# Performance work log

Measured on AMD Instinct MI355X. Metric: run time of the kernel, lower is better.

## Reference

```python
import jax, jax.numpy as jnp
import numpy as np

OUT_F, IN_F = 11008, 4096
GROUP_SIZE = 128
NUM_GROUPS = IN_F // GROUP_SIZE  # 32


def setup_inputs() -> dict:
    key = jax.random.key(0)
    k1, k2, k3, k4 = jax.random.split(key, 4)
    x = jax.random.normal(k1, (2, 2048, IN_F), dtype=jnp.float32)
    # signed 4-bit RTN codes in [-8, 7]
    qweight = jax.random.randint(k2, (OUT_F, IN_F), 0, 16, dtype=jnp.int32) - 8
    # per-group scales (out_features, in_features // group_size)
    scales = jax.random.uniform(k3, (OUT_F, NUM_GROUPS), dtype=jnp.float32) * 0.02 + 1e-3
    bias = jax.random.normal(k4, (OUT_F,), dtype=jnp.float32) * 0.01
    return {"x": x, "qweight": qweight, "scales": scales, "bias": bias}


def reference(x, qweight, scales, bias):
    # RTN dequant: w[o, i] = qweight[o, i] * scales[o, i // group_size]
    w = (qweight.astype(x.dtype).reshape(OUT_F, NUM_GROUPS, GROUP_SIZE)
         * scales[:, :, None]).reshape(OUT_F, IN_F)
    # y = x @ w.T + bias  -> [batch, seq, out_features]
    return jnp.einsum('bsi,oi->bso', x, w) + bias
```

## Files before the change

### kernel.cpp

```cpp
#include <hip/hip_runtime.h>

#define OUT_F 11008
#define IN_F  4096
#define M_TOT 4096
#define BM    256
#define BN    256
#define BK    64
#define NKT   (IN_F / BK)
#define TM_N  (M_TOT / BM)
#define TN_N  (OUT_F / BN)
#define NWG   (TM_N * TN_N)

typedef __bf16 bf16;
typedef __attribute__((ext_vector_type(8))) __bf16 bf16x8;
typedef __attribute__((ext_vector_type(4))) float  floatx4;

#define GLD_LDS16(g, l) __builtin_amdgcn_global_load_lds(                      \
    (const __attribute__((address_space(1))) unsigned int*)(g),                \
    (__attribute__((address_space(3))) unsigned int*)(l), 16, 0, 0)

__global__ __launch_bounds__(256) void dequant_w_kernel(
    const int* __restrict__ qw, const float* __restrict__ sc,
    bf16* __restrict__ w) {
  const int idx  = blockIdx.x * 256 + threadIdx.x;
  const int o    = idx >> 9;
  const int iv   = idx & 511;
  const float s  = sc[o * (IN_F / 128) + (iv >> 4)];
  const int base = idx * 8;
  const int4* p  = (const int4*)(qw + base);
  const int4 q0  = p[0];
  const int4 q1  = p[1];
  bf16x8 v;
  v[0] = (bf16)((float)q0.x * s);
  v[1] = (bf16)((float)q0.y * s);
  v[2] = (bf16)((float)q0.z * s);
  v[3] = (bf16)((float)q0.w * s);
  v[4] = (bf16)((float)q1.x * s);
  v[5] = (bf16)((float)q1.y * s);
  v[6] = (bf16)((float)q1.z * s);
  v[7] = (bf16)((float)q1.w * s);
  *(bf16x8*)(w + base) = v;
}

__global__ __launch_bounds__(256) void cast_x_kernel(
    const float* __restrict__ x, bf16* __restrict__ xb) {
  const int idx  = blockIdx.x * 256 + threadIdx.x;
  const int base = idx * 8;
  const float4* p = (const float4*)(x + base);
  const float4 a = p[0];
  const float4 b = p[1];
  bf16x8 v;
  v[0] = (bf16)a.x; v[1] = (bf16)a.y; v[2] = (bf16)a.z; v[3] = (bf16)a.w;
  v[4] = (bf16)b.x; v[5] = (bf16)b.y; v[6] = (bf16)b.z; v[7] = (bf16)b.w;
  *(bf16x8*)(xb + base) = v;
}

__global__ __launch_bounds__(512, 2) void gemm_bt_bias_kernel(
    const bf16* __restrict__ A, const bf16* __restrict__ B,
    const float* __restrict__ bias, float* __restrict__ C) {
  __shared__ bf16 As[2][2][128 * 64];
  __shared__ bf16 Bs[2][2][128 * 64];

  const int t    = threadIdx.x;
  const int lane = t & 63;
  const int wv   = t >> 6;
  const int wm   = wv >> 2;
  const int wn   = wv & 3;
  const int lr   = lane & 15;
  const int lq   = lane >> 4;

  const int bid = blockIdx.x;
  const int swz = (bid & 7) * (NWG / 8) + (bid >> 3);
  const int bm  = (swz % TM_N) * BM;
  const int bn  = (swz / TM_N) * BN;

  const int sr  = t >> 3;
  const int sc  = t & 7;
  const int scx = (sc ^ (sr & 7)) * 8;
  const bf16* aStg = A + (bm + sr) * IN_F + scx;
  const bf16* bStg = B + (bn + sr) * IN_F + scx;

#define STAGE_A(BUF, H, KT)                                                  \
  { const bf16* g_ = aStg + (H) * 128 * IN_F + (KT) * BK;                    \
    GLD_LDS16(g_, &As[BUF][H][t * 8]);                                       \
    GLD_LDS16(g_ + 64 * IN_F, &As[BUF][H][t * 8 + 4096]); }
#define STAGE_B(BUF, H, KT)                                                  \
  { const bf16* g_ = bStg + (H) * 128 * IN_F + (KT) * BK;                    \
    GLD_LDS16(g_, &Bs[BUF][H][t * 8]);                                       \
    GLD_LDS16(g_ + 64 * IN_F, &Bs[BUF][H][t * 8 + 4096]); }

  const int xsw = (lr & 7) << 4;
  const int c0b = (lq * 16) ^ xsw;
  const int e0  = c0b >> 1;
  const int e1  = (c0b ^ 64) >> 1;

  floatx4 acc[8][4];
#pragma unroll
  for (int i = 0; i < 8; i++)
#pragma unroll
    for (int j = 0; j < 4; j++)
      acc[i][j] = (floatx4){0.f, 0.f, 0.f, 0.f};

  bf16x8 afA[2][2], afB[2][2], bfr[4][2];

#define READ_AF(DST, CURB, I0)                                               \
  { const bf16* aB_ = &As[CURB][wm][0];                                      \
    _Pragma("unroll") for (int ii_ = 0; ii_ < 2; ++ii_) {                    \
      const int row_ = ((I0) + ii_) * 16 + lr;                               \
      DST[ii_][0] = *(const bf16x8*)&aB_[row_ * 64 + e0];                    \
      DST[ii_][1] = *(const bf16x8*)&aB_[row_ * 64 + e1]; } }

#define READ_BF(CURB)                                                        \
  { const bf16* bB_ = &Bs[CURB][wn >> 1][(wn & 1) * (64 * 64)];              \
    _Pragma("unroll") for (int j_ = 0; j_ < 4; ++j_) {                       \
      const int row_ = j_ * 16 + lr;                                         \
      bfr[j_][0] = *(const bf16x8*)&bB_[row_ * 64 + e0];                     \
      bfr[j_][1] = *(const bf16x8*)&bB_[row_ * 64 + e1]; } }

#define MFMA_PH(AFS, I0)                                                     \
  __builtin_amdgcn_s_setprio(1);                                             \
  _Pragma("unroll") for (int ii_ = 0; ii_ < 2; ++ii_)                        \
    _Pragma("unroll") for (int j_ = 0; j_ < 4; ++j_)                         \
      _Pragma("unroll") for (int kk_ = 0; kk_ < 2; ++kk_)                    \
        acc[(I0) + ii_][j_] = __builtin_amdgcn_mfma_f32_16x16x32_bf16(       \
            AFS[ii_][kk_], bfr[j_][kk_], acc[(I0) + ii_][j_], 0, 0, 0);      \
  __builtin_amdgcn_s_setprio(0);

  STAGE_A(0, 0, 0) STAGE_A(0, 1, 0) STAGE_B(0, 0, 0) STAGE_B(0, 1, 0)
  STAGE_B(1, 0, 1) STAGE_B(1, 1, 1)
  asm volatile("s_waitcnt vmcnt(4)" ::: "memory");
  __builtin_amdgcn_s_barrier();
  READ_AF(afA, 0, 0)
  READ_BF(0)

  for (int ktb = 0; ktb < NKT; ktb += 2) {
#define TILE_BODY(CUR, NXT, KT)                                              \
    { const int kt_ = (KT);                                                  \
       \
      READ_AF(afB, CUR, 2)                                                   \
      if (kt_ + 1 < NKT) STAGE_A(NXT, 0, kt_ + 1)                            \
      __builtin_amdgcn_s_barrier();                                          \
      MFMA_PH(afA, 0)                                                        \
      __builtin_amdgcn_s_barrier();                                          \
       \
      READ_AF(afA, CUR, 4)                                                   \
      if (kt_ + 1 < NKT) STAGE_A(NXT, 1, kt_ + 1)                            \
      __builtin_amdgcn_s_barrier();                                          \
      MFMA_PH(afB, 2)                                                        \
      __builtin_amdgcn_s_barrier();                                          \
       \
      READ_AF(afB, CUR, 6)                                                   \
      if (kt_ + 2 < NKT) STAGE_B(CUR, 0, kt_ + 2)                            \
      __builtin_amdgcn_s_barrier();                                          \
      MFMA_PH(afA, 4)                                                        \
      __builtin_amdgcn_s_barrier();                                          \
         \
         \
      if (kt_ + 2 < NKT) {                                                   \
        STAGE_B(CUR, 1, kt_ + 2)                                             \
        asm volatile("s_waitcnt vmcnt(4)" ::: "memory");                     \
      } else {                                                               \
        asm volatile("s_waitcnt vmcnt(0)" ::: "memory");                     \
      }                                                                      \
      __builtin_amdgcn_s_barrier();                                          \
      if (kt_ + 1 < NKT) READ_AF(afA, NXT, 0)                                \
      MFMA_PH(afB, 6)                                                        \
      if (kt_ + 1 < NKT) READ_BF(NXT)                                        \
      __builtin_amdgcn_s_barrier(); }
    TILE_BODY(0, 1, ktb)
    TILE_BODY(1, 0, ktb + 1)
#undef TILE_BODY
  }

#pragma unroll
  for (int j = 0; j < 4; ++j) {
    const int col = bn + wn * 64 + j * 16 + lr;
    const float bv = bias[col];
#pragma unroll
    for (int i = 0; i < 8; ++i) {
      const int row0 = bm + wm * 128 + i * 16 + lq * 4;
#pragma unroll
      for (int r = 0; r < 4; ++r)
        __builtin_nontemporal_store(
            acc[i][j][r] + bv, &C[(size_t)(row0 + r) * OUT_F + col]);
    }
  }
}

extern "C" void kernel_launch(void* const* d_in, const int* in_sizes, int n_in,
                              void* d_out, int out_size, void* d_ws, size_t ws_size,
                              hipStream_t stream) {
  const float* x    = (const float*)d_in[0];
  const int*   qw   = (const int*)d_in[1];
  const float* sc   = (const float*)d_in[2];
  const float* bias = (const float*)d_in[3];
  float* out = (float*)d_out;

  bf16* wq = (bf16*)d_ws;
  bf16* xb = (bf16*)((char*)d_ws + (size_t)OUT_F * IN_F * sizeof(bf16));

  dequant_w_kernel<<<(OUT_F * IN_F / 8) / 256, 256, 0, stream>>>(qw, sc, wq);
  cast_x_kernel<<<(M_TOT * IN_F / 8) / 256, 256, 0, stream>>>(x, xb);

  gemm_bt_bias_kernel<<<dim3(NWG), 512, 0, stream>>>(xb, wq, bias, out);
}
```

Before: 769.1 us.

## Reschedule GEMM staging earlier and split last MFMA phase by k-half

Issues both halves of the next A tile in the first phase and moves B staging one phase earlier, so global-to-LDS loads start sooner. The last MFMA phase is split into two k-halves, and the B fragments for the next tile are read for each half as soon as it is consumed, overlapping LDS reads with MFMA work. The aim is to hide LDS and global latency at the tile boundary. The trade-off is more loads in flight at once and a tighter vmcnt/barrier ordering that must stay correct.

```diff
diff --git a/kernel.cpp b/kernel.cpp
--- a/kernel.cpp
+++ b/kernel.cpp
@@ -110,20 +110,22 @@
       DST[ii_][0] = *(const bf16x8*)&aB_[row_ * 64 + e0];                    \
       DST[ii_][1] = *(const bf16x8*)&aB_[row_ * 64 + e1]; } }
 
-#define READ_BF(CURB)                                                        \
+#define READ_BF_KK(CURB, KK, EK)                                             \
   { const bf16* bB_ = &Bs[CURB][wn >> 1][(wn & 1) * (64 * 64)];              \
     _Pragma("unroll") for (int j_ = 0; j_ < 4; ++j_) {                       \
       const int row_ = j_ * 16 + lr;                                         \
-      bfr[j_][0] = *(const bf16x8*)&bB_[row_ * 64 + e0];                     \
-      bfr[j_][1] = *(const bf16x8*)&bB_[row_ * 64 + e1]; } }
-
-#define MFMA_PH(AFS, I0)                                                     \
-  __builtin_amdgcn_s_setprio(1);                                             \
+      bfr[j_][KK] = *(const bf16x8*)&bB_[row_ * 64 + (EK)]; } }
+
+#define MFMA8(AFS, I0, KK)                                                   \
   _Pragma("unroll") for (int ii_ = 0; ii_ < 2; ++ii_)                        \
     _Pragma("unroll") for (int j_ = 0; j_ < 4; ++j_)                         \
-      _Pragma("unroll") for (int kk_ = 0; kk_ < 2; ++kk_)                    \
-        acc[(I0) + ii_][j_] = __builtin_amdgcn_mfma_f32_16x16x32_bf16(       \
-            AFS[ii_][kk_], bfr[j_][kk_], acc[(I0) + ii_][j_], 0, 0, 0);      \
+      acc[(I0) + ii_][j_] = __builtin_amdgcn_mfma_f32_16x16x32_bf16(         \
+          AFS[ii_][KK], bfr[j_][KK], acc[(I0) + ii_][j_], 0, 0, 0);
+
+#define MFMA16(AFS, I0)                                                      \
+  __builtin_amdgcn_s_setprio(1);                                             \
+  MFMA8(AFS, I0, 1)                                                          \
+  MFMA8(AFS, I0, 0)                                                          \
   __builtin_amdgcn_s_setprio(0);
 
   STAGE_A(0, 0, 0) STAGE_A(0, 1, 0) STAGE_B(0, 0, 0) STAGE_B(0, 1, 0)
@@ -131,41 +133,46 @@
   asm volatile("s_waitcnt vmcnt(4)" ::: "memory");
   __builtin_amdgcn_s_barrier();
   READ_AF(afA, 0, 0)
-  READ_BF(0)
+  READ_BF_KK(0, 1, e1)
+  READ_BF_KK(0, 0, e0)
 
   for (int ktb = 0; ktb < NKT; ktb += 2) {
 #define TILE_BODY(CUR, NXT, KT)                                              \
     { const int kt_ = (KT);                                                  \
-       \
+               \
       READ_AF(afB, CUR, 2)                                                   \
-      if (kt_ + 1 < NKT) STAGE_A(NXT, 0, kt_ + 1)                            \
-      __builtin_amdgcn_s_barrier();                                          \
-      MFMA_PH(afA, 0)                                                        \
-      __builtin_amdgcn_s_barrier();                                          \
-       \
+      if (kt_ + 1 < NKT) { STAGE_A(NXT, 0, kt_ + 1)                          \
+                           STAGE_A(NXT, 1, kt_ + 1) }                        \
+      __builtin_amdgcn_s_barrier();                                          \
+      MFMA16(afA, 0)                                                         \
+      __builtin_amdgcn_s_barrier();                                          \
+                  \
       READ_AF(afA, CUR, 4)                                                   \
-      if (kt_ + 1 < NKT) STAGE_A(NXT, 1, kt_ + 1)                            \
-      __builtin_amdgcn_s_barrier();                                          \
-      MFMA_PH(afB, 2)                                                        \
-      __builtin_amdgcn_s_barrier();                                          \
-       \
+      if (kt_ + 2 < NKT) STAGE_B(CUR, 0, kt_ + 2)                            \
+      __builtin_amdgcn_s_barrier();                                          \
+      MFMA16(afB, 2)                                                         \
+      __builtin_amdgcn_s_barrier();                                          \
+                  \
       READ_AF(afB, CUR, 6)                                                   \
-      if (kt_ + 2 < NKT) STAGE_B(CUR, 0, kt_ + 2)                            \
-      __builtin_amdgcn_s_barrier();                                          \
-      MFMA_PH(afA, 4)                                                        \
-      __builtin_amdgcn_s_barrier();                                          \
-         \
+      if (kt_ + 2 < NKT) STAGE_B(CUR, 1, kt_ + 2)                            \
+      __builtin_amdgcn_s_barrier();                                          \
+      MFMA16(afA, 4)                                                         \
+      __builtin_amdgcn_s_barrier();                                          \
+          \
          \
       if (kt_ + 2 < NKT) {                                                   \
-        STAGE_B(CUR, 1, kt_ + 2)                                             \
         asm volatile("s_waitcnt vmcnt(4)" ::: "memory");                     \
       } else {                                                               \
         asm volatile("s_waitcnt vmcnt(0)" ::: "memory");                     \
       }                                                                      \
       __builtin_amdgcn_s_barrier();                                          \
       if (kt_ + 1 < NKT) READ_AF(afA, NXT, 0)                                \
-      MFMA_PH(afB, 6)                                                        \
-      if (kt_ + 1 < NKT) READ_BF(NXT)                                        \
+      __builtin_amdgcn_s_setprio(1);                                         \
+      MFMA8(afB, 6, 1)                                                       \
+      if (kt_ + 1 < NKT) READ_BF_KK(NXT, 1, e1)                              \
+      MFMA8(afB, 6, 0)                                                       \
+      __builtin_amdgcn_s_setprio(0);                                         \
+      if (kt_ + 1 < NKT) READ_BF_KK(NXT, 0, e0)                              \
       __builtin_amdgcn_s_barrier(); }
     TILE_BODY(0, 1, ktb)
     TILE_BODY(1, 0, ktb + 1)
```

New measurement: 759.2 us. Within noise of the previous version (-1.3%).
